# Kernel optimization log

Hardware: AMD Instinct MI355X
Metric: run time of the kernel (lower is better)

The kernel has to match this reference:

```python
import jax, jax.numpy as jnp
import numpy as np

B, N, C, H = 8192, 36, 128, 8
HD = C // H  # 16
FOCUS = 3
EPS = 1e-4


def setup_inputs() -> dict:
    key = jax.random.key(0)
    ks = jax.random.split(key, 10)
    x = jax.random.normal(ks[0], (B, N, C), dtype=jnp.float32)
    pos = jax.random.normal(ks[1], (B, N, C), dtype=jnp.float32)
    mask = jax.random.randint(ks[2], (B, N), 0, 2).astype(jnp.float32)
    coords = jax.random.randint(ks[3], (B * N, 4), 0, 8).astype(jnp.int64)
    voxel_inds = jax.random.permutation(ks[4], B * N).reshape(B, N).astype(jnp.int64)
    s = 0.02
    qk_w = jax.random.normal(ks[5], (C, 2 * C), dtype=jnp.float32) * s
    qk_b = jnp.zeros((2 * C,), dtype=jnp.float32)
    v_w = jax.random.normal(ks[6], (C, C), dtype=jnp.float32) * s
    v_b = jnp.zeros((C,), dtype=jnp.float32)
    proj_w = jax.random.normal(ks[7], (C, C), dtype=jnp.float32) * s
    proj_b = jnp.zeros((C,), dtype=jnp.float32)
    return {"x": x, "pos": pos, "mask": mask, "qk_w": qk_w, "qk_b": qk_b,
            "v_w": v_w, "v_b": v_b, "proj_w": proj_w, "proj_b": proj_b,
            "coords": coords, "voxel_inds": voxel_inds}


def reference(x, pos, mask, qk_w, qk_b, v_w, v_b, proj_w, proj_b, coords, voxel_inds):
    b, n, c = x.shape
    qk = (x + pos) @ qk_w + qk_b                      # (B,N,2C)
    q, k = qk[..., :c], qk[..., c:]
    v = x @ v_w + v_b                                 # (B,N,C)
    k = k * mask[..., None]
    # split heads -> (B,H,N,HD)
    q = q.reshape(b, n, H, HD).transpose(0, 2, 1, 3)
    k = k.reshape(b, n, H, HD).transpose(0, 2, 1, 3)
    v = v.reshape(b, n, H, HD).transpose(0, 2, 1, 3)
    # focusing power
    q = q ** FOCUS
    k = k ** FOCUS
    # q normalized per-token over channels; k normalized per-channel over tokens
    # (original rearranges k to (bh, c, n) before norm(dim=-1))
    q = q / (EPS + jnp.linalg.norm(q, axis=-1, keepdims=True))
    k = k / (EPS + jnp.linalg.norm(k, axis=2, keepdims=True))
    # linear attention: kv = k^T v (HD x HD), then q @ kv
    kv = jnp.einsum('bhnc,bhnd->bhcd', k, v)          # (B,H,HD,HD)
    out = jnp.einsum('bhnc,bhcd->bhnd', q, kv)        # (B,H,N,HD)
    out = out.transpose(0, 2, 1, 3).reshape(b, n, c)  # (B,N,C)
    num = jnp.sum(mask, axis=-1, keepdims=True)       # (B,1)
    out = out / (num[..., None] + EPS)
    # inverse-permutation gather: perm[voxel_inds.flat] = arange
    flat = voxel_inds.reshape(-1)
    M = coords.shape[0]
    perm = jnp.zeros((M,), dtype=flat.dtype).at[flat].set(
        jnp.arange(M, dtype=flat.dtype))
    out = out.reshape(-1, c)[perm]                    # (M,C)
    out = out @ proj_w + proj_b
    return out
```

## Files before the change

kernel.cpp:

```cpp
#include <hip/hip_runtime.h>

typedef __bf16 bf16x8 __attribute__((ext_vector_type(8)));
typedef float f32x4 __attribute__((ext_vector_type(4)));

#define Bdim 8192
#define Nn 36
#define Cc 128
#define EPSf 1e-4f

#define WS_QK_HI 0
#define WS_QK_LO 32768
#define WS_V_HI  65536
#define WS_P_HI  81920

#define OFF_XH   0
#define OFF_PH   12288
#define OFF_PL   24576
#define OFF_KT   0
#define OFF_VT   12288
#define OFF_QH   24576
#define OFF_KV   33792
#define OFF_O    0
#define OFF_MASK 39936
#define OFF_VOX  40128
#define OFF_INN  40272
#define LDS_BYTES 40448

__device__ inline uint bfh(float f) {
    __bf16 h = (__bf16)f;
    return (uint)(*(const ushort*)&h);
}
__device__ inline uint bfl(float f) {
    float hf = (float)((__bf16)f);
    __bf16 l = (__bf16)(f - hf);
    return (uint)(*(const ushort*)&l);
}
__device__ inline uint pk2h(float a, float b) { return bfh(a) | (bfh(b) << 16); }
__device__ inline uint pk2l(float a, float b) { return bfl(a) | (bfl(b) << 16); }

union U8 { bf16x8 v; uint u[4]; };

__global__ __launch_bounds__(256)
void prep_frags(const float* __restrict__ qk_w, const float* __restrict__ v_w,
                const float* __restrict__ proj_w, ushort* __restrict__ ws)
{
    int e = blockIdx.x * 256 + threadIdx.x;
    const float* W; int N; int idx; int hi_off; int lo_off;
    if (e < 32768)      { W = qk_w;   N = 256; hi_off = WS_QK_HI; lo_off = WS_QK_LO; idx = e; }
    else if (e < 49152) { W = v_w;    N = 128; hi_off = WS_V_HI;  lo_off = -1;       idx = e - 32768; }
    else                { W = proj_w; N = 128; hi_off = WS_P_HI;  lo_off = -1;       idx = e - 49152; }
    int j    = idx & 7;
    int lane = (idx >> 3) & 63;
    int ks   = (idx >> 9) & 3;
    int ct   = idx >> 11;
    int col  = ct * 16 + (lane & 15);
    int k    = ks * 32 + (lane >> 4) * 8 + j;
    float v  = W[k * N + col];
    ws[hi_off + idx] = (ushort)bfh(v);
    if (lo_off >= 0) ws[lo_off + idx] = (ushort)bfl(v);
}

__global__ __launch_bounds__(512, 6)
void fla_mfma(const float* __restrict__ x, const float* __restrict__ pos,
              const float* __restrict__ mask, const float* __restrict__ qk_b,
              const float* __restrict__ v_b, const float* __restrict__ proj_b,
              const int* __restrict__ vox, const ushort* __restrict__ ws,
              float* __restrict__ out)
{
    __shared__ __align__(16) char lds[LDS_BYTES];
    const int t = threadIdx.x;
    const int b = blockIdx.x;
    const int lane = t & 63;
    const int wv = t >> 6;

    const int  rsel = lane & 15;
    const int  grp  = lane >> 4;
    const uint kgrp = (uint)grp * 8u;
    const uint sw   = ((uint)rsel) << 4;

    const float* xg = x + (size_t)b * (Nn * Cc);
    const float* pg = pos + (size_t)b * (Nn * Cc);
    #pragma unroll
    for (int it = 0; it < 3; ++it) {
        int idx = t + it * 512;
        int n = idx >> 5;
        int c4 = (idx & 31) << 2;
        float4 xv = make_float4(0.f, 0.f, 0.f, 0.f);
        float4 pv = make_float4(0.f, 0.f, 0.f, 0.f);
        if (n < Nn) {
            xv = *(const float4*)(xg + n * Cc + c4);
            pv = *(const float4*)(pg + n * Cc + c4);
        }
        float s0 = xv.x + pv.x, s1 = xv.y + pv.y, s2 = xv.z + pv.z, s3 = xv.w + pv.w;
        uint ba = (uint)n * 256u + (((uint)(c4 * 2)) ^ (((uint)n & 15u) << 4));
        *(uint2*)(lds + OFF_XH + ba) = make_uint2(pk2h(xv.x, xv.y), pk2h(xv.z, xv.w));
        *(uint2*)(lds + OFF_PH + ba) = make_uint2(pk2h(s0, s1), pk2h(s2, s3));
        *(uint2*)(lds + OFF_PL + ba) = make_uint2(pk2l(s0, s1), pk2l(s2, s3));
    }
    if (t < 48) ((float*)(lds + OFF_MASK))[t] = (t < Nn) ? mask[(size_t)b * Nn + t] : 0.f;
    if (t >= 64 && t < 64 + Nn) ((int*)(lds + OFF_VOX))[t - 64] = vox[(size_t)b * Nn + (t - 64)];
    if (t == 128) {
        float s = 0.f;
        for (int n = 0; n < Nn; ++n) s += mask[(size_t)b * Nn + n];
        *(float*)(lds + OFF_INN) = 1.f / (s + EPSf);
    }
    __syncthreads();

    f32x4 accV[3];
    f32x4 accQ[3][2];
    #pragma unroll
    for (int rt = 0; rt < 3; ++rt) {
        accV[rt] = (f32x4){0.f, 0.f, 0.f, 0.f};
        accQ[rt][0] = (f32x4){0.f, 0.f, 0.f, 0.f};
        accQ[rt][1] = (f32x4){0.f, 0.f, 0.f, 0.f};
    }
    #pragma unroll
    for (int ks = 0; ks < 4; ++ks) {
        uint ka = (((uint)(ks * 32) + kgrp) * 2u) ^ sw;
        bf16x8 xh[3];
        #pragma unroll
        for (int rt = 0; rt < 3; ++rt)
            xh[rt] = *(const bf16x8*)(lds + OFF_XH + (uint)(rt * 16 + rsel) * 256u + ka);
        int f = ((wv * 4 + ks) * 64 + lane) * 8;
        bf16x8 bvh = *(const bf16x8*)(ws + WS_V_HI + f);
        #pragma unroll
        for (int rt = 0; rt < 3; ++rt)
            accV[rt] = __builtin_amdgcn_mfma_f32_16x16x32_bf16(xh[rt], bvh, accV[rt], 0, 0, 0);
    }
    #pragma unroll
    for (int ks = 0; ks < 4; ++ks) {
        uint ka = (((uint)(ks * 32) + kgrp) * 2u) ^ sw;
        bf16x8 ph[3], pl[3];
        #pragma unroll
        for (int rt = 0; rt < 3; ++rt) {
            uint ba = (uint)(rt * 16 + rsel) * 256u + ka;
            ph[rt] = *(const bf16x8*)(lds + OFF_PH + ba);
            pl[rt] = *(const bf16x8*)(lds + OFF_PL + ba);
        }
        #pragma unroll
        for (int ci = 0; ci < 2; ++ci) {
            int f = (((wv * 2 + ci) * 4 + ks) * 64 + lane) * 8;
            bf16x8 bh = *(const bf16x8*)(ws + WS_QK_HI + f);
            bf16x8 bl = *(const bf16x8*)(ws + WS_QK_LO + f);
            #pragma unroll
            for (int rt = 0; rt < 3; ++rt) {
                accQ[rt][ci] = __builtin_amdgcn_mfma_f32_16x16x32_bf16(ph[rt], bh, accQ[rt][ci], 0, 0, 0);
                accQ[rt][ci] = __builtin_amdgcn_mfma_f32_16x16x32_bf16(ph[rt], bl, accQ[rt][ci], 0, 0, 0);
                accQ[rt][ci] = __builtin_amdgcn_mfma_f32_16x16x32_bf16(pl[rt], bh, accQ[rt][ci], 0, 0, 0);
            }
        }
    }
    __syncthreads();

    const float* sM = (const float*)(lds + OFF_MASK);
    {
        int colv = wv * 16 + rsel;
        float vb = v_b[colv];
        #pragma unroll
        for (int rt = 0; rt < 3; ++rt) {
            float a0 = accV[rt][0] + vb, a1 = accV[rt][1] + vb;
            float a2 = accV[rt][2] + vb, a3 = accV[rt][3] + vb;
            uint addr = OFF_VT + (uint)(colv * 48 + rt * 16 + grp * 4) * 2u;
            *(uint2*)(lds + addr) = make_uint2(pk2h(a0, a1), pk2h(a2, a3));
        }
    }
    if (wv < 4) {
        #pragma unroll
        for (int ci = 0; ci < 2; ++ci) {
            int colq = (wv * 2 + ci) * 16 + rsel;
            float qb = qk_b[colq];
            uint cb2 = (uint)(colq * 2);
            #pragma unroll
            for (int rt = 0; rt < 3; ++rt) {
                #pragma unroll
                for (int r = 0; r < 4; ++r) {
                    int row = rt * 16 + grp * 4 + r;
                    if (row < Nn) {
                        float q1 = accQ[rt][ci][r] + qb;
                        float q3 = q1 * q1 * q1;
                        uint ba = (uint)row * 256u + (cb2 ^ (((uint)row & 15u) << 4));
                        *(ushort*)(lds + OFF_QH + ba) = (ushort)bfh(q3);
                    }
                }
            }
        }
    } else {
        #pragma unroll
        for (int ci = 0; ci < 2; ++ci) {
            int colk = ((wv - 4) * 2 + ci) * 16 + rsel;
            float kb = qk_b[Cc + colk];
            #pragma unroll
            for (int rt = 0; rt < 3; ++rt) {
                float k3v[4];
                #pragma unroll
                for (int r = 0; r < 4; ++r) {
                    int row = rt * 16 + grp * 4 + r;
                    float k1 = (accQ[rt][ci][r] + kb) * sM[row];
                    k3v[r] = k1 * k1 * k1;
                }
                uint addr = OFF_KT + (uint)(colk * 48 + rt * 16 + grp * 4) * 2u;
                *(uint2*)(lds + addr) = make_uint2(pk2h(k3v[0], k3v[1]), pk2h(k3v[2], k3v[3]));
            }
        }
    }
    __syncthreads();

    {
        int col16 = wv * 16 + rsel;
        uint a0 = OFF_KT + (uint)(col16 * 48 + grp * 8) * 2u;
        uint b0 = OFF_VT + (uint)(col16 * 48 + grp * 8) * 2u;
        bf16x8 kA0 = *(const bf16x8*)(lds + a0);
        bf16x8 vB0 = *(const bf16x8*)(lds + b0);
        U8 kA1, vB1;
        kA1.u[0] = kA1.u[1] = kA1.u[2] = kA1.u[3] = 0u;
        vB1.u[0] = vB1.u[1] = vB1.u[2] = vB1.u[3] = 0u;
        if (grp < 2) {
            kA1.v = *(const bf16x8*)(lds + a0 + 64);
            vB1.v = *(const bf16x8*)(lds + b0 + 64);
        }
        float s = 0.f;
        #pragma unroll
        for (int j = 0; j < 8; ++j) { float q = (float)kA0[j]; s += q * q; }
        #pragma unroll
        for (int j = 0; j < 8; ++j) { float q = (float)kA1.v[j]; s += q * q; }
        s += __shfl_xor(s, 16);
        s += __shfl_xor(s, 32);
        float invkn = 1.f / (EPSf + sqrtf(s));

        f32x4 kvacc = (f32x4){0.f, 0.f, 0.f, 0.f};
        kvacc = __builtin_amdgcn_mfma_f32_16x16x32_bf16(kA0, vB0, kvacc, 0, 0, 0);
        kvacc = __builtin_amdgcn_mfma_f32_16x16x32_bf16(kA1.v, vB1.v, kvacc, 0, 0, 0);

        float f0 = __shfl(invkn, grp * 4 + 0);
        float f1 = __shfl(invkn, grp * 4 + 1);
        float f2 = __shfl(invkn, grp * 4 + 2);
        float f3 = __shfl(invkn, grp * 4 + 3);
        uint addr = OFF_KV + (uint)(wv * 384 + rsel * 24 + grp * 4) * 2u;
        *(uint2*)(lds + addr) =
            make_uint2(pk2h(kvacc[0] * f0, kvacc[1] * f1), pk2h(kvacc[2] * f2, kvacc[3] * f3));
    }
    __syncthreads();

    {
        int d = rsel;
        float inn = *(const float*)(lds + OFF_INN);
        U8 bkv;
        bkv.u[0] = bkv.u[1] = bkv.u[2] = bkv.u[3] = 0u;
        if (grp < 2)
            bkv.v = *(const bf16x8*)(lds + OFF_KV + (uint)(wv * 384 + d * 24 + grp * 8) * 2u);
        f32x4 oacc[3];
        float invn[3];
        #pragma unroll
        for (int rt = 0; rt < 3; ++rt) {
            int row = rt * 16 + rsel;
            U8 aq;
            aq.u[0] = aq.u[1] = aq.u[2] = aq.u[3] = 0u;
            if (grp < 2 && row < Nn) {
                uint ba = (uint)row * 256u +
                          (((uint)((wv * 16 + grp * 8) * 2)) ^ (((uint)row & 15u) << 4));
                aq.v = *(const bf16x8*)(lds + OFF_QH + ba);
            }
            float s = 0.f;
            #pragma unroll
            for (int j = 0; j < 8; ++j) { float q = (float)aq.v[j]; s += q * q; }
            s += __shfl_xor(s, 16);
            invn[rt] = 1.f / (EPSf + sqrtf(s));
            f32x4 o = (f32x4){0.f, 0.f, 0.f, 0.f};
            o = __builtin_amdgcn_mfma_f32_16x16x32_bf16(aq.v, bkv.v, o, 0, 0, 0);
            oacc[rt] = o;
        }
        #pragma unroll
        for (int rt = 0; rt < 3; ++rt) {
            #pragma unroll
            for (int r = 0; r < 4; ++r) {
                int rr = grp * 4 + r;
                int row = rt * 16 + rr;
                float fac = __shfl(invn[rt], rr) * inn;
                float val = oacc[rt][r] * fac;
                uint ba = (uint)row * 256u +
                          (((uint)((wv * 16 + d) * 2)) ^ (((uint)row & 15u) << 4));
                *(ushort*)(lds + OFF_O + ba) = (ushort)bfh(val);
            }
        }
    }
    __syncthreads();

    f32x4 accP[3];
    #pragma unroll
    for (int rt = 0; rt < 3; ++rt) accP[rt] = (f32x4){0.f, 0.f, 0.f, 0.f};
    #pragma unroll
    for (int ks = 0; ks < 4; ++ks) {
        uint ka = (((uint)(ks * 32) + kgrp) * 2u) ^ sw;
        bf16x8 oa[3];
        #pragma unroll
        for (int rt = 0; rt < 3; ++rt)
            oa[rt] = *(const bf16x8*)(lds + OFF_O + (uint)(rt * 16 + rsel) * 256u + ka);
        int f = ((wv * 4 + ks) * 64 + lane) * 8;
        bf16x8 bp = *(const bf16x8*)(ws + WS_P_HI + f);
        #pragma unroll
        for (int rt = 0; rt < 3; ++rt)
            accP[rt] = __builtin_amdgcn_mfma_f32_16x16x32_bf16(oa[rt], bp, accP[rt], 0, 0, 0);
    }
    {
        const int* sVx = (const int*)(lds + OFF_VOX);
        int col = wv * 16 + rsel;
        float pb = proj_b[col];
        #pragma unroll
        for (int rt = 0; rt < 3; ++rt) {
            #pragma unroll
            for (int r = 0; r < 4; ++r) {
                int row = rt * 16 + grp * 4 + r;
                if (row < Nn)
                    out[(size_t)sVx[row] * Cc + col] = accP[rt][r] + pb;
            }
        }
    }
}

extern "C" void kernel_launch(void* const* d_in, const int* in_sizes, int n_in,
                              void* d_out, int out_size, void* d_ws, size_t ws_size,
                              hipStream_t stream) {
    (void)in_sizes; (void)n_in; (void)out_size; (void)ws_size;
    const float* x      = (const float*)d_in[0];
    const float* pos    = (const float*)d_in[1];
    const float* mask   = (const float*)d_in[2];
    const float* qk_w   = (const float*)d_in[3];
    const float* qk_b   = (const float*)d_in[4];
    const float* v_w    = (const float*)d_in[5];
    const float* v_b    = (const float*)d_in[6];
    const float* proj_w = (const float*)d_in[7];
    const float* proj_b = (const float*)d_in[8];
    const int*   vox    = (const int*)d_in[10];
    ushort* ws = (ushort*)d_ws;
    float* outp = (float*)d_out;

    hipLaunchKernelGGL(prep_frags, dim3(256), dim3(256), 0, stream, qk_w, v_w, proj_w, ws);
    hipLaunchKernelGGL(fla_mfma, dim3(Bdim), dim3(512), 0, stream,
                       x, pos, mask, qk_b, v_b, proj_b, vox, ws, outp);
}
```

Baseline: 218.9 us.

## Process four batches per block as 144 dense rows to remove padding

Each workgroup now handles four batch elements, stacked as 144 rows (9 full 16-row MFMA tiles) instead of 36 rows padded to 48. This drops the wasted padded MFMA work and lets each wave reuse its weight fragments across four batches. The LDS layout is rebuilt and grows to about 160KB, so only one or two blocks fit per CU, with more registers for 9-tile accumulators. The grid shrinks to B/4 blocks, and the per-batch kv/out stages loop over the four batches.

After: 220.8 us. No clear change (+0.9%).

```diff
diff --git a/kernel.cpp b/kernel.cpp
--- a/kernel.cpp
+++ b/kernel.cpp
@@ -5,6 +5,7 @@
 
 #define Bdim 8192
 #define Nn 36
+#define Mrows 144
 #define Cc 128
 #define EPSf 1e-4f
 
@@ -13,18 +14,16 @@
 #define WS_V_HI  65536
 #define WS_P_HI  81920
 
-#define OFF_XH   0
-#define OFF_PH   12288
-#define OFF_PL   24576
+#define OFF_PH   0
+#define OFF_PL   36864
 #define OFF_KT   0
-#define OFF_VT   12288
-#define OFF_QH   24576
-#define OFF_KV   33792
-#define OFF_O    0
-#define OFF_MASK 39936
-#define OFF_VOX  40128
-#define OFF_INN  40272
-#define LDS_BYTES 40448
+#define OFF_KV   51712
+#define OFF_XH   73728
+#define OFF_QO   73728
+#define OFF_VT   110592
+#define OFF_MASK 162304
+#define OFF_INN  162880
+#define LDS_BYTES 162896
 
 __device__ inline uint bfh(float f) {
     __bf16 h = (__bf16)f;
@@ -39,6 +38,8 @@
 __device__ inline uint pk2l(float a, float b) { return bfl(a) | (bfl(b) << 16); }
 
 union U8 { bf16x8 v; uint u[4]; };
+
+__device__ __forceinline__ int rdiv36(int row) { return (row * 1821) >> 16; }
 
 __global__ __launch_bounds__(256)
 void prep_frags(const float* __restrict__ qk_w, const float* __restrict__ v_w,
@@ -60,7 +61,7 @@
     if (lo_off >= 0) ws[lo_off + idx] = (ushort)bfl(v);
 }
 
-__global__ __launch_bounds__(512, 6)
+__global__ __launch_bounds__(512, 2)
 void fla_mfma(const float* __restrict__ x, const float* __restrict__ pos,
               const float* __restrict__ mask, const float* __restrict__ qk_b,
               const float* __restrict__ v_b, const float* __restrict__ proj_b,
@@ -69,249 +70,270 @@
 {
     __shared__ __align__(16) char lds[LDS_BYTES];
     const int t = threadIdx.x;
-    const int b = blockIdx.x;
     const int lane = t & 63;
     const int wv = t >> 6;
-
     const int  rsel = lane & 15;
     const int  grp  = lane >> 4;
     const uint kgrp = (uint)grp * 8u;
     const uint sw   = ((uint)rsel) << 4;
-
-    const float* xg = x + (size_t)b * (Nn * Cc);
-    const float* pg = pos + (size_t)b * (Nn * Cc);
+    const int base4 = blockIdx.x * 4;
+
+    {
+        const float* xg = x + (size_t)base4 * (Nn * Cc);
+        const float* pg = pos + (size_t)base4 * (Nn * Cc);
+        #pragma unroll
+        for (int it = 0; it < 9; ++it) {
+            int idx = t + it * 512;
+            int n = idx >> 5;
+            int c4 = (idx & 31) << 2;
+            float4 xv = *(const float4*)(xg + n * Cc + c4);
+            float4 pv = *(const float4*)(pg + n * Cc + c4);
+            float s0 = xv.x + pv.x, s1 = xv.y + pv.y;
+            float s2 = xv.z + pv.z, s3 = xv.w + pv.w;
+            uint ba = (uint)n * 256u + (((uint)(c4 * 2)) ^ (((uint)n & 15u) << 4));
+            *(uint2*)(lds + OFF_XH + ba) = make_uint2(pk2h(xv.x, xv.y), pk2h(xv.z, xv.w));
+            *(uint2*)(lds + OFF_PH + ba) = make_uint2(pk2h(s0, s1), pk2h(s2, s3));
+            *(uint2*)(lds + OFF_PL + ba) = make_uint2(pk2l(s0, s1), pk2l(s2, s3));
+        }
+        if (t < Mrows) {
+            int b = rdiv36(t), rl = t - b * 36;
+            ((float*)(lds + OFF_MASK))[t] = mask[(size_t)(base4 + b) * Nn + rl];
+        }
+        if (wv < 4) {
+            float s = (lane < Nn) ? mask[(size_t)(base4 + wv) * Nn + lane] : 0.f;
+            s += __shfl_xor(s, 1);  s += __shfl_xor(s, 2);
+            s += __shfl_xor(s, 4);  s += __shfl_xor(s, 8);
+            s += __shfl_xor(s, 16); s += __shfl_xor(s, 32);
+            if (lane == 0) ((float*)(lds + OFF_INN))[wv] = 1.f / (s + EPSf);
+        }
+    }
+    __syncthreads();
+
+    f32x4 accQ[9][2];
+    f32x4 accV[9];
     #pragma unroll
-    for (int it = 0; it < 3; ++it) {
-        int idx = t + it * 512;
-        int n = idx >> 5;
-        int c4 = (idx & 31) << 2;
-        float4 xv = make_float4(0.f, 0.f, 0.f, 0.f);
-        float4 pv = make_float4(0.f, 0.f, 0.f, 0.f);
-        if (n < Nn) {
-            xv = *(const float4*)(xg + n * Cc + c4);
-            pv = *(const float4*)(pg + n * Cc + c4);
-        }
-        float s0 = xv.x + pv.x, s1 = xv.y + pv.y, s2 = xv.z + pv.z, s3 = xv.w + pv.w;
-        uint ba = (uint)n * 256u + (((uint)(c4 * 2)) ^ (((uint)n & 15u) << 4));
-        *(uint2*)(lds + OFF_XH + ba) = make_uint2(pk2h(xv.x, xv.y), pk2h(xv.z, xv.w));
-        *(uint2*)(lds + OFF_PH + ba) = make_uint2(pk2h(s0, s1), pk2h(s2, s3));
-        *(uint2*)(lds + OFF_PL + ba) = make_uint2(pk2l(s0, s1), pk2l(s2, s3));
-    }
-    if (t < 48) ((float*)(lds + OFF_MASK))[t] = (t < Nn) ? mask[(size_t)b * Nn + t] : 0.f;
-    if (t >= 64 && t < 64 + Nn) ((int*)(lds + OFF_VOX))[t - 64] = vox[(size_t)b * Nn + (t - 64)];
-    if (t == 128) {
-        float s = 0.f;
-        for (int n = 0; n < Nn; ++n) s += mask[(size_t)b * Nn + n];
-        *(float*)(lds + OFF_INN) = 1.f / (s + EPSf);
-    }
-    __syncthreads();
-
-    f32x4 accV[3];
-    f32x4 accQ[3][2];
-    #pragma unroll
-    for (int rt = 0; rt < 3; ++rt) {
-        accV[rt] = (f32x4){0.f, 0.f, 0.f, 0.f};
-        accQ[rt][0] = (f32x4){0.f, 0.f, 0.f, 0.f};
-        accQ[rt][1] = (f32x4){0.f, 0.f, 0.f, 0.f};
+    for (int m = 0; m < 9; ++m) {
+        accQ[m][0] = (f32x4){0.f, 0.f, 0.f, 0.f};
+        accQ[m][1] = (f32x4){0.f, 0.f, 0.f, 0.f};
+        accV[m]    = (f32x4){0.f, 0.f, 0.f, 0.f};
     }
     #pragma unroll
     for (int ks = 0; ks < 4; ++ks) {
         uint ka = (((uint)(ks * 32) + kgrp) * 2u) ^ sw;
-        bf16x8 xh[3];
-        #pragma unroll
-        for (int rt = 0; rt < 3; ++rt)
-            xh[rt] = *(const bf16x8*)(lds + OFF_XH + (uint)(rt * 16 + rsel) * 256u + ka);
-        int f = ((wv * 4 + ks) * 64 + lane) * 8;
-        bf16x8 bvh = *(const bf16x8*)(ws + WS_V_HI + f);
-        #pragma unroll
-        for (int rt = 0; rt < 3; ++rt)
-            accV[rt] = __builtin_amdgcn_mfma_f32_16x16x32_bf16(xh[rt], bvh, accV[rt], 0, 0, 0);
+        int f0 = (((wv * 2 + 0) * 4 + ks) * 64 + lane) * 8;
+        int f1 = (((wv * 2 + 1) * 4 + ks) * 64 + lane) * 8;
+        bf16x8 bh0 = *(const bf16x8*)(ws + WS_QK_HI + f0);
+        bf16x8 bl0 = *(const bf16x8*)(ws + WS_QK_LO + f0);
+        bf16x8 bh1 = *(const bf16x8*)(ws + WS_QK_HI + f1);
+        bf16x8 bl1 = *(const bf16x8*)(ws + WS_QK_LO + f1);
+        #pragma unroll
+        for (int m = 0; m < 9; ++m) {
+            uint ba = (uint)(m * 16 + rsel) * 256u + ka;
+            bf16x8 ph = *(const bf16x8*)(lds + OFF_PH + ba);
+            bf16x8 pl = *(const bf16x8*)(lds + OFF_PL + ba);
+            accQ[m][0] = __builtin_amdgcn_mfma_f32_16x16x32_bf16(ph, bh0, accQ[m][0], 0, 0, 0);
+            accQ[m][0] = __builtin_amdgcn_mfma_f32_16x16x32_bf16(ph, bl0, accQ[m][0], 0, 0, 0);
+            accQ[m][0] = __builtin_amdgcn_mfma_f32_16x16x32_bf16(pl, bh0, accQ[m][0], 0, 0, 0);
+            accQ[m][1] = __builtin_amdgcn_mfma_f32_16x16x32_bf16(ph, bh1, accQ[m][1], 0, 0, 0);
+            accQ[m][1] = __builtin_amdgcn_mfma_f32_16x16x32_bf16(ph, bl1, accQ[m][1], 0, 0, 0);
+            accQ[m][1] = __builtin_amdgcn_mfma_f32_16x16x32_bf16(pl, bh1, accQ[m][1], 0, 0, 0);
+        }
     }
     #pragma unroll
     for (int ks = 0; ks < 4; ++ks) {
         uint ka = (((uint)(ks * 32) + kgrp) * 2u) ^ sw;
-        bf16x8 ph[3], pl[3];
-        #pragma unroll
-        for (int rt = 0; rt < 3; ++rt) {
-            uint ba = (uint)(rt * 16 + rsel) * 256u + ka;
-            ph[rt] = *(const bf16x8*)(lds + OFF_PH + ba);
-            pl[rt] = *(const bf16x8*)(lds + OFF_PL + ba);
-        }
-        #pragma unroll
-        for (int ci = 0; ci < 2; ++ci) {
-            int f = (((wv * 2 + ci) * 4 + ks) * 64 + lane) * 8;
-            bf16x8 bh = *(const bf16x8*)(ws + WS_QK_HI + f);
-            bf16x8 bl = *(const bf16x8*)(ws + WS_QK_LO + f);
+        int fv = ((wv * 4 + ks) * 64 + lane) * 8;
+        bf16x8 bv = *(const bf16x8*)(ws + WS_V_HI + fv);
+        #pragma unroll
+        for (int m = 0; m < 9; ++m) {
+            uint ba = (uint)(m * 16 + rsel) * 256u + ka;
+            bf16x8 xh = *(const bf16x8*)(lds + OFF_XH + ba);
+            accV[m] = __builtin_amdgcn_mfma_f32_16x16x32_bf16(xh, bv, accV[m], 0, 0, 0);
+        }
+    }
+    __syncthreads();
+
+    {
+        const float* sM = (const float*)(lds + OFF_MASK);
+        {
+            int colv = wv * 16 + rsel;
+            float vb = v_b[colv];
+            #pragma unroll
+            for (int m = 0; m < 9; ++m) {
+                int row0 = m * 16 + grp * 4;
+                int b = rdiv36(row0), rl = row0 - b * 36;
+                float a0 = accV[m][0] + vb, a1 = accV[m][1] + vb;
+                float a2 = accV[m][2] + vb, a3 = accV[m][3] + vb;
+                uint addr = OFF_VT + (uint)(colv * 202 + b * 50 + rl) * 2u;
+                *(uint2*)(lds + addr) = make_uint2(pk2h(a0, a1), pk2h(a2, a3));
+            }
+        }
+        if (wv < 4) {
+            #pragma unroll
+            for (int ci = 0; ci < 2; ++ci) {
+                int colq = (wv * 2 + ci) * 16 + rsel;
+                float qb = qk_b[colq];
+                uint cb2 = (uint)(colq * 2);
+                #pragma unroll
+                for (int m = 0; m < 9; ++m) {
+                    #pragma unroll
+                    for (int r = 0; r < 4; ++r) {
+                        int row = m * 16 + grp * 4 + r;
+                        float q1 = accQ[m][ci][r] + qb;
+                        float q3 = q1 * q1 * q1;
+                        uint ba = (uint)row * 256u + (cb2 ^ (((uint)row & 15u) << 4));
+                        *(ushort*)(lds + OFF_QO + ba) = (ushort)bfh(q3);
+                    }
+                }
+            }
+        } else {
+            #pragma unroll
+            for (int ci = 0; ci < 2; ++ci) {
+                int colk = ((wv - 4) * 2 + ci) * 16 + rsel;
+                float kb = qk_b[Cc + colk];
+                #pragma unroll
+                for (int m = 0; m < 9; ++m) {
+                    int row0 = m * 16 + grp * 4;
+                    int b = rdiv36(row0), rl = row0 - b * 36;
+                    float k3v[4];
+                    #pragma unroll
+                    for (int r = 0; r < 4; ++r) {
+                        float k1 = (accQ[m][ci][r] + kb) * sM[row0 + r];
+                        k3v[r] = k1 * k1 * k1;
+                    }
+                    uint addr = OFF_KT + (uint)(colk * 202 + b * 50 + rl) * 2u;
+                    *(uint2*)(lds + addr) = make_uint2(pk2h(k3v[0], k3v[1]), pk2h(k3v[2], k3v[3]));
+                }
+            }
+        }
+        {
+            int col = t >> 2, b = t & 3;
+            uint pbase = (uint)(col * 202 + b * 50 + 36) * 2u;
+            #pragma unroll
+            for (int j = 0; j < 7; ++j) {
+                *(uint*)(lds + OFF_KT + pbase + j * 4) = 0u;
+                *(uint*)(lds + OFF_VT + pbase + j * 4) = 0u;
+            }
+        }
+    }
+    __syncthreads();
+
+    {
+        int col16 = wv * 16 + rsel;
+        #pragma unroll
+        for (int b = 0; b < 4; ++b) {
+            uint a0 = OFF_KT + (uint)(col16 * 202 + b * 50 + grp * 8) * 2u;
+            uint b0 = OFF_VT + (uint)(col16 * 202 + b * 50 + grp * 8) * 2u;
+            bf16x8 kA0 = *(const bf16x8*)(lds + a0);
+            bf16x8 vB0 = *(const bf16x8*)(lds + b0);
+            U8 kA1, vB1;
+            kA1.u[0] = kA1.u[1] = kA1.u[2] = kA1.u[3] = 0u;
+            vB1.u[0] = vB1.u[1] = vB1.u[2] = vB1.u[3] = 0u;
+            if (grp < 2) {
+                kA1.v = *(const bf16x8*)(lds + a0 + 64);
+                vB1.v = *(const bf16x8*)(lds + b0 + 64);
+            }
+            float s = 0.f;
+            #pragma unroll
+            for (int j = 0; j < 8; ++j) { float q = (float)kA0[j]; s += q * q; }
+            #pragma unroll
+            for (int j = 0; j < 8; ++j) { float q = (float)kA1.v[j]; s += q * q; }
+            s += __shfl_xor(s, 16);
+            s += __shfl_xor(s, 32);
+            float invkn = 1.f / (EPSf + sqrtf(s));
+
+            f32x4 kvacc = (f32x4){0.f, 0.f, 0.f, 0.f};
+            kvacc = __builtin_amdgcn_mfma_f32_16x16x32_bf16(kA0, vB0, kvacc, 0, 0, 0);
+            kvacc = __builtin_amdgcn_mfma_f32_16x16x32_bf16(kA1.v, vB1.v, kvacc, 0, 0, 0);
+
+            float f0 = __shfl(invkn, grp * 4 + 0);
+            float f1 = __shfl(invkn, grp * 4 + 1);
+            float f2 = __shfl(invkn, grp * 4 + 2);
+            float f3 = __shfl(invkn, grp * 4 + 3);
+            uint addr = OFF_KV + (uint)((((b * 8 + wv) * 16 + rsel) * 16) + grp * 4) * 2u;
+            *(uint2*)(lds + addr) =
+                make_uint2(pk2h(kvacc[0] * f0, kvacc[1] * f1), pk2h(kvacc[2] * f2, kvacc[3] * f3));
+        }
+    }
+
+    {
+        #pragma unroll
+        for (int b = 0; b < 4; ++b) {
+            U8 bkv;
+            bkv.u[0] = bkv.u[1] = bkv.u[2] = bkv.u[3] = 0u;
+            if (grp < 2)
+                bkv.v = *(const bf16x8*)(lds + OFF_KV +
+                          (uint)((((b * 8 + wv) * 16 + rsel) * 16) + grp * 8) * 2u);
+            float inn = ((const float*)(lds + OFF_INN))[b];
+            f32x4 oacc[3];
+            float invn[3];
             #pragma unroll
             for (int rt = 0; rt < 3; ++rt) {
-                accQ[rt][ci] = __builtin_amdgcn_mfma_f32_16x16x32_bf16(ph[rt], bh, accQ[rt][ci], 0, 0, 0);
-                accQ[rt][ci] = __builtin_amdgcn_mfma_f32_16x16x32_bf16(ph[rt], bl, accQ[rt][ci], 0, 0, 0);
-                accQ[rt][ci] = __builtin_amdgcn_mfma_f32_16x16x32_bf16(pl[rt], bh, accQ[rt][ci], 0, 0, 0);
-            }
-        }
-    }
-    __syncthreads();
-
-    const float* sM = (const float*)(lds + OFF_MASK);
-    {
-        int colv = wv * 16 + rsel;
-        float vb = v_b[colv];
-        #pragma unroll
-        for (int rt = 0; rt < 3; ++rt) {
-            float a0 = accV[rt][0] + vb, a1 = accV[rt][1] + vb;
-            float a2 = accV[rt][2] + vb, a3 = accV[rt][3] + vb;
-            uint addr = OFF_VT + (uint)(colv * 48 + rt * 16 + grp * 4) * 2u;
-            *(uint2*)(lds + addr) = make_uint2(pk2h(a0, a1), pk2h(a2, a3));
-        }
-    }
-    if (wv < 4) {
-        #pragma unroll
-        for (int ci = 0; ci < 2; ++ci) {
-            int colq = (wv * 2 + ci) * 16 + rsel;
-            float qb = qk_b[colq];
-            uint cb2 = (uint)(colq * 2);
+                int rloc = rt * 16 + rsel;
+                U8 aq;
+                aq.u[0] = aq.u[1] = aq.u[2] = aq.u[3] = 0u;
+                if (grp < 2 && rloc < Nn) {
+                    int rg = b * 36 + rloc;
+                    uint ba = (uint)rg * 256u +
+                              (((uint)(wv * 32 + grp * 16)) ^ (((uint)rg & 15u) << 4));
+                    aq.v = *(const bf16x8*)(lds + OFF_QO + ba);
+                }
+                float s = 0.f;
+                #pragma unroll
+                for (int j = 0; j < 8; ++j) { float q = (float)aq.v[j]; s += q * q; }
+                s += __shfl_xor(s, 16);
+                invn[rt] = 1.f / (EPSf + sqrtf(s));
+                f32x4 o = (f32x4){0.f, 0.f, 0.f, 0.f};
+                o = __builtin_amdgcn_mfma_f32_16x16x32_bf16(aq.v, bkv.v, o, 0, 0, 0);
+                oacc[rt] = o;
+            }
             #pragma unroll
             for (int rt = 0; rt < 3; ++rt) {
                 #pragma unroll
                 for (int r = 0; r < 4; ++r) {
-                    int row = rt * 16 + grp * 4 + r;
-                    if (row < Nn) {
-                        float q1 = accQ[rt][ci][r] + qb;
-                        float q3 = q1 * q1 * q1;
-                        uint ba = (uint)row * 256u + (cb2 ^ (((uint)row & 15u) << 4));
-                        *(ushort*)(lds + OFF_QH + ba) = (ushort)bfh(q3);
+                    int rr = grp * 4 + r;
+                    int rloc = rt * 16 + rr;
+                    if (rloc < Nn) {
+                        int rg = b * 36 + rloc;
+                        float fac = __shfl(invn[rt], rr) * inn;
+                        float val = oacc[rt][r] * fac;
+                        uint ba = (uint)rg * 256u +
+                                  (((uint)((wv * 16 + rsel) * 2)) ^ (((uint)rg & 15u) << 4));
+                        *(ushort*)(lds + OFF_QO + ba) = (ushort)bfh(val);
                     }
                 }
             }
         }
-    } else {
-        #pragma unroll
-        for (int ci = 0; ci < 2; ++ci) {
-            int colk = ((wv - 4) * 2 + ci) * 16 + rsel;
-            float kb = qk_b[Cc + colk];
-            #pragma unroll
-            for (int rt = 0; rt < 3; ++rt) {
-                float k3v[4];
-                #pragma unroll
-                for (int r = 0; r < 4; ++r) {
-                    int row = rt * 16 + grp * 4 + r;
-                    float k1 = (accQ[rt][ci][r] + kb) * sM[row];
-                    k3v[r] = k1 * k1 * k1;
-                }
-                uint addr = OFF_KT + (uint)(colk * 48 + rt * 16 + grp * 4) * 2u;
-                *(uint2*)(lds + addr) = make_uint2(pk2h(k3v[0], k3v[1]), pk2h(k3v[2], k3v[3]));
-            }
-        }
     }
     __syncthreads();
 
     {
-        int col16 = wv * 16 + rsel;
-        uint a0 = OFF_KT + (uint)(col16 * 48 + grp * 8) * 2u;
-        uint b0 = OFF_VT + (uint)(col16 * 48 + grp * 8) * 2u;
-        bf16x8 kA0 = *(const bf16x8*)(lds + a0);
-        bf16x8 vB0 = *(const bf16x8*)(lds + b0);
-        U8 kA1, vB1;
-        kA1.u[0] = kA1.u[1] = kA1.u[2] = kA1.u[3] = 0u;
-        vB1.u[0] = vB1.u[1] = vB1.u[2] = vB1.u[3] = 0u;
-        if (grp < 2) {
-            kA1.v = *(const bf16x8*)(lds + a0 + 64);
-            vB1.v = *(const bf16x8*)(lds + b0 + 64);
-        }
-        float s = 0.f;
-        #pragma unroll
-        for (int j = 0; j < 8; ++j) { float q = (float)kA0[j]; s += q * q; }
-        #pragma unroll
-        for (int j = 0; j < 8; ++j) { float q = (float)kA1.v[j]; s += q * q; }
-        s += __shfl_xor(s, 16);
-        s += __shfl_xor(s, 32);
-        float invkn = 1.f / (EPSf + sqrtf(s));
-
-        f32x4 kvacc = (f32x4){0.f, 0.f, 0.f, 0.f};
-        kvacc = __builtin_amdgcn_mfma_f32_16x16x32_bf16(kA0, vB0, kvacc, 0, 0, 0);
-        kvacc = __builtin_amdgcn_mfma_f32_16x16x32_bf16(kA1.v, vB1.v, kvacc, 0, 0, 0);
-
-        float f0 = __shfl(invkn, grp * 4 + 0);
-        float f1 = __shfl(invkn, grp * 4 + 1);
-        float f2 = __shfl(invkn, grp * 4 + 2);
-        float f3 = __shfl(invkn, grp * 4 + 3);
-        uint addr = OFF_KV + (uint)(wv * 384 + rsel * 24 + grp * 4) * 2u;
-        *(uint2*)(lds + addr) =
-            make_uint2(pk2h(kvacc[0] * f0, kvacc[1] * f1), pk2h(kvacc[2] * f2, kvacc[3] * f3));
-    }
-    __syncthreads();
-
-    {
-        int d = rsel;
-        float inn = *(const float*)(lds + OFF_INN);
-        U8 bkv;
-        bkv.u[0] = bkv.u[1] = bkv.u[2] = bkv.u[3] = 0u;
-        if (grp < 2)
-            bkv.v = *(const bf16x8*)(lds + OFF_KV + (uint)(wv * 384 + d * 24 + grp * 8) * 2u);
-        f32x4 oacc[3];
-        float invn[3];
-        #pragma unroll
-        for (int rt = 0; rt < 3; ++rt) {
-            int row = rt * 16 + rsel;
-            U8 aq;
-            aq.u[0] = aq.u[1] = aq.u[2] = aq.u[3] = 0u;
-            if (grp < 2 && row < Nn) {
-                uint ba = (uint)row * 256u +
-                          (((uint)((wv * 16 + grp * 8) * 2)) ^ (((uint)row & 15u) << 4));
-                aq.v = *(const bf16x8*)(lds + OFF_QH + ba);
-            }
-            float s = 0.f;
-            #pragma unroll
-            for (int j = 0; j < 8; ++j) { float q = (float)aq.v[j]; s += q * q; }
-            s += __shfl_xor(s, 16);
-            invn[rt] = 1.f / (EPSf + sqrtf(s));
-            f32x4 o = (f32x4){0.f, 0.f, 0.f, 0.f};
-            o = __builtin_amdgcn_mfma_f32_16x16x32_bf16(aq.v, bkv.v, o, 0, 0, 0);
-            oacc[rt] = o;
-        }
-        #pragma unroll
-        for (int rt = 0; rt < 3; ++rt) {
-            #pragma unroll
-            for (int r = 0; r < 4; ++r) {
-                int rr = grp * 4 + r;
-                int row = rt * 16 + rr;
-                float fac = __shfl(invn[rt], rr) * inn;
-                float val = oacc[rt][r] * fac;
-                uint ba = (uint)row * 256u +
-                          (((uint)((wv * 16 + d) * 2)) ^ (((uint)row & 15u) << 4));
-                *(ushort*)(lds + OFF_O + ba) = (ushort)bfh(val);
-            }
-        }
-    }
-    __syncthreads();
-
-    f32x4 accP[3];
-    #pragma unroll
-    for (int rt = 0; rt < 3; ++rt) accP[rt] = (f32x4){0.f, 0.f, 0.f, 0.f};
-    #pragma unroll
-    for (int ks = 0; ks < 4; ++ks) {
-        uint ka = (((uint)(ks * 32) + kgrp) * 2u) ^ sw;
-        bf16x8 oa[3];
-        #pragma unroll
-        for (int rt = 0; rt < 3; ++rt)
-            oa[rt] = *(const bf16x8*)(lds + OFF_O + (uint)(rt * 16 + rsel) * 256u + ka);
-        int f = ((wv * 4 + ks) * 64 + lane) * 8;
-        bf16x8 bp = *(const bf16x8*)(ws + WS_P_HI + f);
-        #pragma unroll
-        for (int rt = 0; rt < 3; ++rt)
-            accP[rt] = __builtin_amdgcn_mfma_f32_16x16x32_bf16(oa[rt], bp, accP[rt], 0, 0, 0);
-    }
-    {
-        const int* sVx = (const int*)(lds + OFF_VOX);
+        f32x4 accP[9];
+        #pragma unroll
+        for (int m = 0; m < 9; ++m) accP[m] = (f32x4){0.f, 0.f, 0.f, 0.f};
+        #pragma unroll
+        for (int ks = 0; ks < 4; ++ks) {
+            uint ka = (((uint)(ks * 32) + kgrp) * 2u) ^ sw;
+            int fp = ((wv * 4 + ks) * 64 + lane) * 8;
+            bf16x8 bp = *(const bf16x8*)(ws + WS_P_HI + fp);
+            #pragma unroll
+            for (int m = 0; m < 9; ++m) {
+                uint ba = (uint)(m * 16 + rsel) * 256u + ka;
+                bf16x8 oa = *(const bf16x8*)(lds + OFF_QO + ba);
+                accP[m] = __builtin_amdgcn_mfma_f32_16x16x32_bf16(oa, bp, accP[m], 0, 0, 0);
+            }
+        }
         int col = wv * 16 + rsel;
         float pb = proj_b[col];
         #pragma unroll
-        for (int rt = 0; rt < 3; ++rt) {
+        for (int m = 0; m < 9; ++m) {
+            int row0 = m * 16 + grp * 4;
+            int b = rdiv36(row0), rl = row0 - b * 36;
+            const int* voxb = vox + (size_t)(base4 + b) * Nn + rl;
             #pragma unroll
             for (int r = 0; r < 4; ++r) {
-                int row = rt * 16 + grp * 4 + r;
-                if (row < Nn)
-                    out[(size_t)sVx[row] * Cc + col] = accP[rt][r] + pb;
+                int vrow = voxb[r];
+                out[(size_t)vrow * Cc + col] = accP[m][r] + pb;
             }
         }
     }
@@ -335,6 +357,6 @@
     float* outp = (float*)d_out;
 
     hipLaunchKernelGGL(prep_frags, dim3(256), dim3(256), 0, stream, qk_w, v_w, proj_w, ws);
-    hipLaunchKernelGGL(fla_mfma, dim3(Bdim), dim3(512), 0, stream,
+    hipLaunchKernelGGL(fla_mfma, dim3(Bdim / 4), dim3(512), 0, stream,
                        x, pos, mask, qk_b, v_b, proj_b, vox, ws, outp);
 }
```
